# Kernel tuning notes

Hardware: AMD Instinct MI355X
Metric: run time of the kernel (lower is better)

## Reference

```python
import jax, jax.numpy as jnp
import numpy as np

N = 30000      # nodes
K = 32         # in-degree per node (before self loop)
NFEAT = 512
NHID = 128
NCLASS = 64


def setup_inputs() -> dict:
    key = jax.random.key(0)
    k1, k2, k3, k4 = jax.random.split(key, 4)
    x = jax.random.normal(k1, (N, NFEAT), dtype=jnp.float32)
    # neighbor offsets in [0, N-2]; src = (dst + off + 1) % N guarantees src != dst
    neighbors = jax.random.randint(k2, (N, K), 0, N - 1)
    W1 = jax.random.normal(k3, (NFEAT, NHID), dtype=jnp.float32) / np.float32(np.sqrt(NFEAT))
    b1 = jnp.zeros((NHID,), dtype=jnp.float32)
    W2 = jax.random.normal(k4, (NHID, NCLASS), dtype=jnp.float32) / np.float32(np.sqrt(NHID))
    b2 = jnp.zeros((NCLASS,), dtype=jnp.float32)
    return {"x": x, "neighbors": neighbors, "W1": W1, "b1": b1, "W2": W2, "b2": b2}


def _median_conv(x, nbrs_all, W, b):
    # x: [N, Fin]; nbrs_all: [N, D] neighbor indices (self loop included)
    h = x @ W                          # [N, Fout]
    gathered = h[nbrs_all]             # [N, D, Fout]
    d = nbrs_all.shape[1]
    # torch .median(dim=1) returns the lower median: sorted index (d-1)//2
    med = jnp.sort(gathered, axis=1)[:, (d - 1) // 2]  # [N, Fout]
    return med + b


def reference(x, neighbors, W1, b1, W2, b2):
    n = x.shape[0]
    dst = jnp.arange(n)
    src = (dst[:, None] + neighbors + 1) % n            # no self loops (remove_self_loops)
    nbrs_all = jnp.concatenate([src, dst[:, None]], axis=1)  # add_self_loops -> degree K+1
    # dropout is identity at eval time
    h = jax.nn.relu(_median_conv(x, nbrs_all, W1, b1))
    out = _median_conv(h, nbrs_all, W2, b2)
    return jax.nn.log_softmax(out, axis=1)
```

## Files before the change

### kernel.cpp

```cpp
#include <hip/hip_runtime.h>
#include <hip/hip_bf16.h>
#include <math.h>

static constexpr int NN = 30000;
static constexpr int NF = 512;
static constexpr int NH = 128;
static constexpr int NC = 64;

typedef unsigned int uint32;

__device__ __forceinline__ float bf_lo(uint32 p) { return __uint_as_float(p << 16); }
__device__ __forceinline__ float bf_hi(uint32 p) { return __uint_as_float(p & 0xffff0000u); }

__device__ __forceinline__ void cswap(float& a, float& b) {
  float lo = fminf(a, b), hi = fmaxf(a, b);
  a = lo; b = hi;
}

__device__ __forceinline__ void medsel32(float v[32], float& m15, float& m16) {
  #pragma unroll
  for (int k = 2; k <= 16; k <<= 1) {
    #pragma unroll
    for (int j = k >> 1; j > 0; j >>= 1) {
      #pragma unroll
      for (int h = 0; h < 2; ++h) {
        #pragma unroll
        for (int i = 0; i < 16; ++i) {
          const int l = i ^ j;
          if (l > i) {
            const int a = h * 16 + i, b = h * 16 + l;
            if ((i & k) == 0) cswap(v[a], v[b]);
            else              cswap(v[b], v[a]);
          }
        }
      }
    }
  }
  m15 = fminf(v[0], v[31]);
  m16 = fmaxf(v[0], v[31]);
  #pragma unroll
  for (int i = 1; i < 16; ++i) {
    m15 = fmaxf(m15, fminf(v[i], v[31 - i]));
    m16 = fminf(m16, fmaxf(v[i], v[31 - i]));
  }
}

__global__ __launch_bounds__(256) void k1_gemm1(const float* __restrict__ x,
                                                const float* __restrict__ W1,
                                                __hip_bfloat16* __restrict__ h0b) {
  __shared__ float As[32][132];
  __shared__ float Bs[32][128];
  const int tid = threadIdx.x;
  const int m0  = blockIdx.x * 128;
  const int tr  = tid >> 4;
  const int tc  = tid & 15;

  float acc[8][8];
  #pragma unroll
  for (int r = 0; r < 8; ++r)
    #pragma unroll
    for (int c = 0; c < 8; ++c) acc[r][c] = 0.f;

  for (int k0 = 0; k0 < NF; k0 += 32) {
    #pragma unroll
    for (int it = 0; it < 4; ++it) {
      const int p   = tid + it * 256;
      const int row = p >> 3;
      const int c4  = p & 7;
      int gr = m0 + row;
      if (gr >= NN) gr = NN - 1;
      const float4 a = *reinterpret_cast<const float4*>(&x[(size_t)gr * NF + k0 + c4 * 4]);
      As[c4 * 4 + 0][row] = a.x;
      As[c4 * 4 + 1][row] = a.y;
      As[c4 * 4 + 2][row] = a.z;
      As[c4 * 4 + 3][row] = a.w;
    }
    #pragma unroll
    for (int it = 0; it < 4; ++it) {
      const int p   = tid + it * 256;
      const int row = p >> 5;
      const int c4  = p & 31;
      *reinterpret_cast<float4*>(&Bs[row][c4 * 4]) =
          *reinterpret_cast<const float4*>(&W1[(k0 + row) * NH + c4 * 4]);
    }
    __syncthreads();

    #pragma unroll
    for (int kk = 0; kk < 32; ++kk) {
      const float4 a0 = *reinterpret_cast<const float4*>(&As[kk][tr * 8 + 0]);
      const float4 a1 = *reinterpret_cast<const float4*>(&As[kk][tr * 8 + 4]);
      const float4 b0 = *reinterpret_cast<const float4*>(&Bs[kk][tc * 8 + 0]);
      const float4 b1 = *reinterpret_cast<const float4*>(&Bs[kk][tc * 8 + 4]);
      const float av[8] = {a0.x, a0.y, a0.z, a0.w, a1.x, a1.y, a1.z, a1.w};
      const float bv[8] = {b0.x, b0.y, b0.z, b0.w, b1.x, b1.y, b1.z, b1.w};
      #pragma unroll
      for (int r = 0; r < 8; ++r)
        #pragma unroll
        for (int c = 0; c < 8; ++c)
          acc[r][c] = fmaf(av[r], bv[c], acc[r][c]);
    }
    __syncthreads();
  }

  #pragma unroll
  for (int r = 0; r < 8; ++r) {
    const int gr = m0 + tr * 8 + r;
    if (gr < NN) {
      alignas(16) __hip_bfloat16 t[8];
      #pragma unroll
      for (int c = 0; c < 8; ++c) t[c] = __float2bfloat16(acc[r][c]);
      *reinterpret_cast<uint4*>(&h0b[(size_t)gr * NH + tc * 8]) =
          *reinterpret_cast<const uint4*>(t);
    }
  }
}

__global__ __launch_bounds__(256) void k2_median1_gemm2(const __hip_bfloat16* __restrict__ h0b,
                                                        const int* __restrict__ nbr,
                                                        const float* __restrict__ b1,
                                                        const float* __restrict__ W2,
                                                        __hip_bfloat16* __restrict__ zb) {
  __shared__ int   nb[4][32];
  __shared__ float hs[4][NH];
  const int tid  = threadIdx.x;
  const int g    = tid >> 6;
  const int lane = tid & 63;
  const int i    = blockIdx.x * 4 + g;

  if (lane < 32) nb[g][lane] = nbr[i * 32 + lane];
  __syncthreads();

  const uint32* hrow = reinterpret_cast<const uint32*>(h0b);
  uint32 pr[32];
  #pragma unroll
  for (int k = 0; k < 32; ++k) {
    int idx = i + nb[g][k] + 1;
    if (idx >= NN) idx -= NN;
    pr[k] = hrow[idx * 64 + lane];
  }
  const uint32 ps = hrow[i * 64 + lane];

  float v[32], m15, m16;
  #pragma unroll
  for (int k = 0; k < 32; ++k) v[k] = bf_lo(pr[k]);
  medsel32(v, m15, m16);
  const float hA = fmaxf(fminf(fmaxf(bf_lo(ps), m15), m16) + b1[lane * 2 + 0], 0.f);

  #pragma unroll
  for (int k = 0; k < 32; ++k) v[k] = bf_hi(pr[k]);
  medsel32(v, m15, m16);
  const float hB = fmaxf(fminf(fmaxf(bf_hi(ps), m15), m16) + b1[lane * 2 + 1], 0.f);

  hs[g][lane * 2 + 0] = hA;
  hs[g][lane * 2 + 1] = hB;
  __syncthreads();

  float acc = 0.f;
  #pragma unroll 16
  for (int kk = 0; kk < NH; ++kk)
    acc = fmaf(hs[g][kk], W2[kk * NC + lane], acc);
  zb[i * NC + lane] = __float2bfloat16(acc);
}

__global__ __launch_bounds__(256) void k3_median2_lsm(const __hip_bfloat16* __restrict__ zb,
                                                      const int* __restrict__ nbr,
                                                      const float* __restrict__ b2,
                                                      float* __restrict__ out) {
  __shared__ int nb[8][32];
  const int tid  = threadIdx.x;
  const int g    = tid >> 5;
  const int lane = tid & 31;
  const int i    = blockIdx.x * 8 + g;

  nb[g][lane] = nbr[i * 32 + lane];
  __syncthreads();

  const uint32* zrow = reinterpret_cast<const uint32*>(zb);
  uint32 pr[32];
  #pragma unroll
  for (int k = 0; k < 32; ++k) {
    int idx = i + nb[g][k] + 1;
    if (idx >= NN) idx -= NN;
    pr[k] = zrow[idx * 32 + lane];
  }
  const uint32 ps = zrow[i * 32 + lane];

  float v[32], m15, m16;
  #pragma unroll
  for (int k = 0; k < 32; ++k) v[k] = bf_lo(pr[k]);
  medsel32(v, m15, m16);
  const float oA = fminf(fmaxf(bf_lo(ps), m15), m16) + b2[lane * 2 + 0];

  #pragma unroll
  for (int k = 0; k < 32; ++k) v[k] = bf_hi(pr[k]);
  medsel32(v, m15, m16);
  const float oB = fminf(fmaxf(bf_hi(ps), m15), m16) + b2[lane * 2 + 1];

  float m = fmaxf(oA, oB);
  #pragma unroll
  for (int d = 1; d < 32; d <<= 1) m = fmaxf(m, __shfl_xor(m, d, 32));
  float s = __expf(oA - m) + __expf(oB - m);
  #pragma unroll
  for (int d = 1; d < 32; d <<= 1) s += __shfl_xor(s, d, 32);
  const float ls = __logf(s);

  *reinterpret_cast<float2*>(&out[i * NC + lane * 2]) =
      make_float2(oA - m - ls, oB - m - ls);
}

extern "C" void kernel_launch(void* const* d_in, const int* in_sizes, int n_in,
                              void* d_out, int out_size, void* d_ws, size_t ws_size,
                              hipStream_t stream) {
  const float* x   = (const float*)d_in[0];
  const int*   nbr = (const int*)d_in[1];
  const float* W1  = (const float*)d_in[2];
  const float* b1  = (const float*)d_in[3];
  const float* W2  = (const float*)d_in[4];
  const float* b2  = (const float*)d_in[5];
  float* outp = (float*)d_out;

  __hip_bfloat16* h0b = (__hip_bfloat16*)d_ws;
  __hip_bfloat16* zb  = (__hip_bfloat16*)((char*)d_ws + (size_t)NN * NH * 2);

  k1_gemm1<<<(NN + 127) / 128, 256, 0, stream>>>(x, W1, h0b);
  k2_median1_gemm2<<<NN / 4, 256, 0, stream>>>(h0b, nbr, b1, W2, zb);
  k3_median2_lsm<<<NN / 8, 256, 0, stream>>>(zb, nbr, b2, outp);
}
```

Baseline: 254.8 us.

## Use bf16 MFMA for first GEMM with prepacked W1 layout

Replaces the fp32 shared-memory tiled FMA GEMM for x@W1 with a bf16 MFMA 16x16x32 kernel. A new prep kernel converts W1 to bf16 and repacks it into the MFMA operand layout, and each wave loads its x rows straight from global memory and converts them to bf16 in registers. This removes the FP32 ALU bottleneck of the first GEMM, at the cost of rounding x and W1 to bf16, an extra kernel launch, and scattered 2-byte output stores.

Measured after the change: 212.7 us. 1.2x faster.

```diff
diff --git a/kernel.cpp b/kernel.cpp
--- a/kernel.cpp
+++ b/kernel.cpp
@@ -8,9 +8,16 @@
 static constexpr int NC = 64;
 
 typedef unsigned int uint32;
+typedef __attribute__((ext_vector_type(8))) short bf16x8;
+typedef __attribute__((ext_vector_type(4))) float f32x4;
 
 __device__ __forceinline__ float bf_lo(uint32 p) { return __uint_as_float(p << 16); }
 __device__ __forceinline__ float bf_hi(uint32 p) { return __uint_as_float(p & 0xffff0000u); }
+
+__device__ __forceinline__ unsigned short bfbits(float f) {
+  __hip_bfloat16 h = __float2bfloat16(f);
+  return *reinterpret_cast<unsigned short*>(&h);
+}
 
 __device__ __forceinline__ void cswap(float& a, float& b) {
   float lo = fminf(a, b), hi = fmaxf(a, b);
@@ -45,72 +52,64 @@
   }
 }
 
+__global__ __launch_bounds__(256) void k0_prepW1(const float* __restrict__ W1,
+                                                 unsigned short* __restrict__ Bp) {
+  const int g  = blockIdx.x * 256 + threadIdx.x;
+  const int kt = g >> 9;
+  const int r  = g & 511;
+  const int nt = r >> 6;
+  const int l  = r & 63;
+  const int ks = l >> 4;
+  const int ct = l & 15;
+  alignas(16) unsigned short t[8];
+  #pragma unroll
+  for (int j = 0; j < 8; ++j)
+    t[j] = bfbits(W1[(kt * 32 + ks * 8 + j) * NH + nt * 16 + ct]);
+  *reinterpret_cast<uint4*>(&Bp[(size_t)g * 8]) = *reinterpret_cast<const uint4*>(t);
+}
+
 __global__ __launch_bounds__(256) void k1_gemm1(const float* __restrict__ x,
-                                                const float* __restrict__ W1,
+                                                const unsigned short* __restrict__ Bp,
                                                 __hip_bfloat16* __restrict__ h0b) {
-  __shared__ float As[32][132];
-  __shared__ float Bs[32][128];
   const int tid = threadIdx.x;
-  const int m0  = blockIdx.x * 128;
-  const int tr  = tid >> 4;
-  const int tc  = tid & 15;
-
-  float acc[8][8];
-  #pragma unroll
-  for (int r = 0; r < 8; ++r)
+  const int w   = tid >> 6;
+  const int l   = tid & 63;
+  const int m0  = blockIdx.x * 64 + w * 16;
+
+  int arow = m0 + (l & 15);
+  if (arow >= NN) arow = NN - 1;
+  const float* xrow = x + (size_t)arow * NF + (l >> 4) * 8;
+
+  f32x4 acc[8];
+  #pragma unroll
+  for (int nt = 0; nt < 8; ++nt) acc[nt] = (f32x4){0.f, 0.f, 0.f, 0.f};
+
+  #pragma unroll 2
+  for (int kt = 0; kt < 16; ++kt) {
+    const float4 a0 = *reinterpret_cast<const float4*>(xrow + kt * 32);
+    const float4 a1 = *reinterpret_cast<const float4*>(xrow + kt * 32 + 4);
+    union { bf16x8 v; unsigned short u[8]; } A;
+    const float av[8] = {a0.x, a0.y, a0.z, a0.w, a1.x, a1.y, a1.z, a1.w};
     #pragma unroll
-    for (int c = 0; c < 8; ++c) acc[r][c] = 0.f;
-
-  for (int k0 = 0; k0 < NF; k0 += 32) {
+    for (int j = 0; j < 8; ++j) A.u[j] = bfbits(av[j]);
+
+    const unsigned short* bbase = Bp + (size_t)kt * 4096 + l * 8;
     #pragma unroll
-    for (int it = 0; it < 4; ++it) {
-      const int p   = tid + it * 256;
-      const int row = p >> 3;
-      const int c4  = p & 7;
-      int gr = m0 + row;
-      if (gr >= NN) gr = NN - 1;
-      const float4 a = *reinterpret_cast<const float4*>(&x[(size_t)gr * NF + k0 + c4 * 4]);
-      As[c4 * 4 + 0][row] = a.x;
-      As[c4 * 4 + 1][row] = a.y;
-      As[c4 * 4 + 2][row] = a.z;
-      As[c4 * 4 + 3][row] = a.w;
+    for (int nt = 0; nt < 8; ++nt) {
+      const bf16x8 B = *reinterpret_cast<const bf16x8*>(bbase + nt * 512);
+      acc[nt] = __builtin_amdgcn_mfma_f32_16x16x32_bf16(A.v, B, acc[nt], 0, 0, 0);
     }
-    #pragma unroll
-    for (int it = 0; it < 4; ++it) {
-      const int p   = tid + it * 256;
-      const int row = p >> 5;
-      const int c4  = p & 31;
-      *reinterpret_cast<float4*>(&Bs[row][c4 * 4]) =
-          *reinterpret_cast<const float4*>(&W1[(k0 + row) * NH + c4 * 4]);
-    }
-    __syncthreads();
-
-    #pragma unroll
-    for (int kk = 0; kk < 32; ++kk) {
-      const float4 a0 = *reinterpret_cast<const float4*>(&As[kk][tr * 8 + 0]);
-      const float4 a1 = *reinterpret_cast<const float4*>(&As[kk][tr * 8 + 4]);
-      const float4 b0 = *reinterpret_cast<const float4*>(&Bs[kk][tc * 8 + 0]);
-      const float4 b1 = *reinterpret_cast<const float4*>(&Bs[kk][tc * 8 + 4]);
-      const float av[8] = {a0.x, a0.y, a0.z, a0.w, a1.x, a1.y, a1.z, a1.w};
-      const float bv[8] = {b0.x, b0.y, b0.z, b0.w, b1.x, b1.y, b1.z, b1.w};
+  }
+
+  const int rbase = m0 + (l >> 4) * 4;
+  const int cbase = l & 15;
+  #pragma unroll
+  for (int q = 0; q < 4; ++q) {
+    const int rr = rbase + q;
+    if (rr < NN) {
       #pragma unroll
-      for (int r = 0; r < 8; ++r)
-        #pragma unroll
-        for (int c = 0; c < 8; ++c)
-          acc[r][c] = fmaf(av[r], bv[c], acc[r][c]);
-    }
-    __syncthreads();
-  }
-
-  #pragma unroll
-  for (int r = 0; r < 8; ++r) {
-    const int gr = m0 + tr * 8 + r;
-    if (gr < NN) {
-      alignas(16) __hip_bfloat16 t[8];
-      #pragma unroll
-      for (int c = 0; c < 8; ++c) t[c] = __float2bfloat16(acc[r][c]);
-      *reinterpret_cast<uint4*>(&h0b[(size_t)gr * NH + tc * 8]) =
-          *reinterpret_cast<const uint4*>(t);
+      for (int nt = 0; nt < 8; ++nt)
+        h0b[(size_t)rr * NH + nt * 16 + cbase] = __float2bfloat16(acc[nt][q]);
     }
   }
 }
@@ -221,8 +220,10 @@
 
   __hip_bfloat16* h0b = (__hip_bfloat16*)d_ws;
   __hip_bfloat16* zb  = (__hip_bfloat16*)((char*)d_ws + (size_t)NN * NH * 2);
-
-  k1_gemm1<<<(NN + 127) / 128, 256, 0, stream>>>(x, W1, h0b);
+  unsigned short* Bp  = (unsigned short*)((char*)d_ws + (size_t)NN * (NH + NC) * 2);
+
+  k0_prepW1<<<32, 256, 0, stream>>>(W1, Bp);
+  k1_gemm1<<<(NN + 63) / 64, 256, 0, stream>>>(x, Bp, h0b);
   k2_median1_gemm2<<<NN / 4, 256, 0, stream>>>(h0b, nbr, b1, W2, zb);
   k3_median2_lsm<<<NN / 8, 256, 0, stream>>>(zb, nbr, b2, outp);
 }
```
